# Kernel optimization log

Hardware: AMD Instinct MI355X
Metric: run time of the kernel (lower is better)

## Reference

```python
import jax, jax.numpy as jnp
import numpy as np

B, S, C, H, D = 4, 2048, 512, 8, 64
EPS = 1e-5
SCALE = D ** -0.5


def layer_norm(x, w, b):
    m = jnp.mean(x, axis=-1, keepdims=True)
    v = jnp.var(x, axis=-1, keepdims=True)
    return (x - m) * jax.lax.rsqrt(v + EPS) * w + b


def setup_inputs() -> dict:
    key = jax.random.key(0)
    ks = jax.random.split(key, 7)
    s = 0.02
    return {
        "x": jax.random.normal(ks[0], (B, S, C), jnp.float32),
        "Wq": jax.random.normal(ks[1], (C, H * D), jnp.float32) * s,
        "Wk": jax.random.normal(ks[2], (C, H * D), jnp.float32) * s,
        "Wv": jax.random.normal(ks[3], (C, H * D), jnp.float32) * s,
        "Wo": jax.random.normal(ks[4], (H * D, C), jnp.float32) * s,
        "ln1_w": jnp.ones((C,), jnp.float32), "ln1_b": jnp.zeros((C,), jnp.float32),
        "ff_ln1_w": jnp.ones((C,), jnp.float32), "ff_ln1_b": jnp.zeros((C,), jnp.float32),
        "ff_w1": jax.random.normal(ks[5], (C, C), jnp.float32) * s, "ff_b1": jnp.zeros((C,), jnp.float32),
        "ff_ln2_w": jnp.ones((C,), jnp.float32), "ff_ln2_b": jnp.zeros((C,), jnp.float32),
        "ff_w2": jax.random.normal(ks[6], (C, C), jnp.float32) * s, "ff_b2": jnp.zeros((C,), jnp.float32),
        "ln2_w": jnp.ones((C,), jnp.float32), "ln2_b": jnp.zeros((C,), jnp.float32),
    }


def causal_attention(x, Wq, Wk, Wv, Wo):
    # Mathematically identical to the bucketed memory-efficient attention:
    # online-softmax bucketing changes compute order, not the result.
    q = (x @ Wq).reshape(B, S, H, D).transpose(0, 2, 1, 3)  # [B,H,S,D]
    k = (x @ Wk).reshape(B, S, H, D).transpose(0, 2, 1, 3)
    v = (x @ Wv).reshape(B, S, H, D).transpose(0, 2, 1, 3)
    scores = jnp.einsum('bhqd,bhkd->bhqk', q, k) * SCALE  # [B,H,S,S]
    causal = jnp.tril(jnp.ones((S, S), bool))
    scores = jnp.where(causal, scores, jnp.finfo(scores.dtype).min)
    attn = jax.nn.softmax(scores, axis=-1)
    out = jnp.einsum('bhqk,bhkd->bhqd', attn, v)
    out = out.transpose(0, 2, 1, 3).reshape(B, S, H * D)
    return out @ Wo


def reference(x, Wq, Wk, Wv, Wo, ln1_w, ln1_b, ff_ln1_w, ff_ln1_b, ff_w1, ff_b1,
              ff_ln2_w, ff_ln2_b, ff_w2, ff_b2, ln2_w, ln2_b):
    a = causal_attention(x, Wq, Wk, Wv, Wo)
    x_ln = layer_norm(a + x, ln1_w, ln1_b)
    h = layer_norm(x_ln, ff_ln1_w, ff_ln1_b) @ ff_w1 + ff_b1
    h = layer_norm(h, ff_ln2_w, ff_ln2_b) @ ff_w2 + ff_b2
    return layer_norm(h + x_ln, ln2_w, ln2_b)
```

## Files before the change

kernel.cpp:

```cpp
#include <hip/hip_runtime.h>

#define B_ 4
#define S_ 2048
#define C_ 512
#define H_ 8
#define D_ 64
#define M_ 8192

typedef short s8v __attribute__((ext_vector_type(8)));
typedef short s4v __attribute__((ext_vector_type(4)));
typedef float f4v __attribute__((ext_vector_type(4)));
typedef unsigned short u16;
typedef unsigned int u32;

__device__ __forceinline__ u16 f2b(float f) {
    u32 u = __builtin_bit_cast(u32, f);
    u = u + 0x7fffu + ((u >> 16) & 1u);
    return (u16)(u >> 16);
}

__device__ __forceinline__ void b2f8(const s8v v, float* f) {
    #pragma unroll
    for (int k = 0; k < 8; ++k)
        f[k] = __builtin_bit_cast(float, (u32)(u16)v[k] << 16);
}

__device__ __forceinline__ void gl2lds16(const void* g, void* l) {
    __builtin_amdgcn_global_load_lds(
        (const __attribute__((address_space(1))) void*)g,
        (__attribute__((address_space(3))) void*)l, 16, 0, 0);
}

__global__ __launch_bounds__(256) void conv_k(const float* __restrict__ s,
                                              u16* __restrict__ d) {
    const int i = (blockIdx.x * 256 + threadIdx.x) * 4;
    const float4 v = *(const float4*)&s[i];
    ushort4 o;
    o.x = f2b(v.x); o.y = f2b(v.y); o.z = f2b(v.z); o.w = f2b(v.w);
    *(ushort4*)&d[i] = o;
}

__global__ __launch_bounds__(256) void trconv6_k(const float* __restrict__ s0,
                                                 const float* __restrict__ s1,
                                                 const float* __restrict__ s2,
                                                 const float* __restrict__ s3,
                                                 const float* __restrict__ s4,
                                                 const float* __restrict__ s5,
                                                 u16* __restrict__ d0,
                                                 u16* __restrict__ d1,
                                                 u16* __restrict__ d2,
                                                 u16* __restrict__ d3,
                                                 u16* __restrict__ d4,
                                                 u16* __restrict__ d5)
{
    const float* W; u16* Wt;
    switch (blockIdx.z) {
        case 0: W = s0; Wt = d0; break;
        case 1: W = s1; Wt = d1; break;
        case 2: W = s2; Wt = d2; break;
        case 3: W = s3; Wt = d3; break;
        case 4: W = s4; Wt = d4; break;
        default: W = s5; Wt = d5; break;
    }
    __shared__ float t[32][33];
    const int tx = threadIdx.x & 31, ty = threadIdx.x >> 5;
    const int n0 = blockIdx.x * 32, k0 = blockIdx.y * 32;
    #pragma unroll
    for (int i = 0; i < 4; ++i)
        t[ty + i * 8][tx] = W[(size_t)(k0 + ty + i * 8) * C_ + n0 + tx];
    __syncthreads();
    #pragma unroll
    for (int i = 0; i < 4; ++i)
        Wt[(size_t)(n0 + ty + i * 8) * C_ + k0 + tx] = f2b(t[tx][ty + i * 8]);
}

template <bool OB>
__global__ __launch_bounds__(256) void gemm_k(const u16* __restrict__ A,
                                              const u16* __restrict__ Bt,
                                              const float* __restrict__ bias,
                                              void* __restrict__ outv)
{
    __shared__ u16 As[2][4][16][32];
    __shared__ u16 Bs[2][4][16][32];
    const int tid = threadIdx.x;
    const int lane = tid & 63, w = tid >> 6;
    const int q4 = lane >> 4, l16 = lane & 15;
    const int wr = w >> 1, wc = w & 1;
    const int bm = blockIdx.y * 64, bn = blockIdx.x * 64;
    const int lr = lane >> 2, lc = (lane & 3) * 8;

    f4v acc[2][2];
    #pragma unroll
    for (int i = 0; i < 2; ++i)
        #pragma unroll
        for (int j = 0; j < 2; ++j) acc[i][j] = (f4v){0.f, 0.f, 0.f, 0.f};

    gl2lds16(A  + (size_t)(bm + w * 16 + lr) * C_ + lc, (char*)As + w * 1024);
    gl2lds16(Bt + (size_t)(bn + w * 16 + lr) * C_ + lc, (char*)Bs + w * 1024);

    for (int kt = 0; kt < 16; ++kt) {
        __syncthreads();
        const int buf = kt & 1;
        if (kt < 15) {
            const int nb = buf ^ 1, k0 = (kt + 1) * 32;
            gl2lds16(A  + (size_t)(bm + w * 16 + lr) * C_ + k0 + lc,
                     (char*)As + nb * 4096 + w * 1024);
            gl2lds16(Bt + (size_t)(bn + w * 16 + lr) * C_ + k0 + lc,
                     (char*)Bs + nb * 4096 + w * 1024);
        }
        s8v a[2], bfr[2];
        #pragma unroll
        for (int i = 0; i < 2; ++i) {
            const int row = wr * 32 + i * 16 + l16;
            a[i] = *(const s8v*)&As[buf][row >> 4][row & 15][q4 * 8];
        }
        #pragma unroll
        for (int j = 0; j < 2; ++j) {
            const int row = wc * 32 + j * 16 + l16;
            bfr[j] = *(const s8v*)&Bs[buf][row >> 4][row & 15][q4 * 8];
        }
        #pragma unroll
        for (int i = 0; i < 2; ++i)
            #pragma unroll
            for (int j = 0; j < 2; ++j)
                acc[i][j] = __builtin_amdgcn_mfma_f32_16x16x32_bf16(a[i], bfr[j], acc[i][j], 0, 0, 0);
    }

    #pragma unroll
    for (int j = 0; j < 2; ++j) {
        const int n = bn + wc * 32 + j * 16 + l16;
        const float bj = bias ? bias[n] : 0.0f;
        #pragma unroll
        for (int i = 0; i < 2; ++i) {
            const int m = bm + wr * 32 + i * 16 + q4 * 4;
            #pragma unroll
            for (int reg = 0; reg < 4; ++reg) {
                const float vv = acc[i][j][reg] + bj;
                if constexpr (OB) ((u16*)outv)[(size_t)(m + reg) * C_ + n] = f2b(vv);
                else              ((float*)outv)[(size_t)(m + reg) * C_ + n] = vv;
            }
        }
    }
}

__global__ __launch_bounds__(256) void qkv_k(const u16* __restrict__ A,
                                             const u16* __restrict__ Wq,
                                             const u16* __restrict__ Wk,
                                             const u16* __restrict__ Wv,
                                             u16* __restrict__ oq,
                                             u16* __restrict__ ok,
                                             u16* __restrict__ ovt)
{
    __shared__ u16 As[2][4][16][32];
    __shared__ u16 Bs[2][4][16][32];
    const int tid = threadIdx.x;
    const int lane = tid & 63, w = tid >> 6;
    const int q4 = lane >> 4, l16 = lane & 15;
    const int wr = w >> 1, wc = w & 1;
    const int nt = blockIdx.x, which = nt >> 3;
    const u16* Bt = which == 0 ? Wq : (which == 1 ? Wk : Wv);
    const int bm = blockIdx.y * 64, bn = (nt & 7) * 64;
    const int lr = lane >> 2, lc = (lane & 3) * 8;

    f4v acc[2][2];
    #pragma unroll
    for (int i = 0; i < 2; ++i)
        #pragma unroll
        for (int j = 0; j < 2; ++j) acc[i][j] = (f4v){0.f, 0.f, 0.f, 0.f};

    gl2lds16(A  + (size_t)(bm + w * 16 + lr) * C_ + lc, (char*)As + w * 1024);
    gl2lds16(Bt + (size_t)(bn + w * 16 + lr) * C_ + lc, (char*)Bs + w * 1024);

    for (int kt = 0; kt < 16; ++kt) {
        __syncthreads();
        const int buf = kt & 1;
        if (kt < 15) {
            const int nb = buf ^ 1, k0 = (kt + 1) * 32;
            gl2lds16(A  + (size_t)(bm + w * 16 + lr) * C_ + k0 + lc,
                     (char*)As + nb * 4096 + w * 1024);
            gl2lds16(Bt + (size_t)(bn + w * 16 + lr) * C_ + k0 + lc,
                     (char*)Bs + nb * 4096 + w * 1024);
        }
        s8v a[2], bfr[2];
        #pragma unroll
        for (int i = 0; i < 2; ++i) {
            const int row = wr * 32 + i * 16 + l16;
            a[i] = *(const s8v*)&As[buf][row >> 4][row & 15][q4 * 8];
        }
        #pragma unroll
        for (int j = 0; j < 2; ++j) {
            const int row = wc * 32 + j * 16 + l16;
            bfr[j] = *(const s8v*)&Bs[buf][row >> 4][row & 15][q4 * 8];
        }
        #pragma unroll
        for (int i = 0; i < 2; ++i)
            #pragma unroll
            for (int j = 0; j < 2; ++j)
                acc[i][j] = __builtin_amdgcn_mfma_f32_16x16x32_bf16(a[i], bfr[j], acc[i][j], 0, 0, 0);
    }

    if (which == 0) {
        #pragma unroll
        for (int j = 0; j < 2; ++j) {
            const int n = bn + wc * 32 + j * 16 + l16;
            #pragma unroll
            for (int i = 0; i < 2; ++i) {
                const int m = bm + wr * 32 + i * 16 + q4 * 4;
                #pragma unroll
                for (int reg = 0; reg < 4; ++reg)
                    oq[(size_t)(m + reg) * C_ + n] = f2b(acc[i][j][reg]);
            }
        }
    } else if (which == 1) {
        #pragma unroll
        for (int j = 0; j < 2; ++j) {
            const int n = bn + wc * 32 + j * 16 + l16;
            const int nswz = (n & ~31) | ((((n >> 3) & 3) ^ q4) << 3) | (n & 7);
            #pragma unroll
            for (int i = 0; i < 2; ++i) {
                const int m = bm + wr * 32 + i * 16 + q4 * 4;
                #pragma unroll
                for (int reg = 0; reg < 4; ++reg)
                    ok[(size_t)(m + reg) * C_ + nswz] = f2b(acc[i][j][reg]);
            }
        }
    } else {
        const int bglob = bm >> 11;
        const int sbase = bm & (S_ - 1);
        #pragma unroll
        for (int j = 0; j < 2; ++j) {
            const int n = bn + wc * 32 + j * 16 + l16;
            const int h = n >> 6, d = n & 63;
            u16* vrow = ovt + ((size_t)(bglob * H_ + h) * D_ + d) * S_;
            const int xw = d & 7;
            #pragma unroll
            for (int i = 0; i < 2; ++i) {
                const int s = sbase + wr * 32 + i * 16 + q4 * 4;
                const int pg = ((s & 31) >> 2) ^ xw;
                s4v pv;
                #pragma unroll
                for (int reg = 0; reg < 4; ++reg) pv[reg] = (short)f2b(acc[i][j][reg]);
                *(s4v*)&vrow[(s & ~31) + (pg << 2)] = pv;
            }
        }
    }
}

__global__ __launch_bounds__(256) void ln2xb_k(const u16* __restrict__ in,
                                               const float* __restrict__ res,
                                               const float* __restrict__ w1,
                                               const float* __restrict__ b1,
                                               const float* __restrict__ w2,
                                               const float* __restrict__ b2,
                                               u16* __restrict__ out1,
                                               u16* __restrict__ out2)
{
    const int lane = threadIdx.x & 63;
    const int row  = blockIdx.x * 4 + (threadIdx.x >> 6);
    const size_t off = (size_t)row * C_ + lane * 8;
    float v[8];
    b2f8(*(const s8v*)&in[off], v);
    {
        const float4 r0 = *(const float4*)&res[off];
        const float4 r1 = *(const float4*)&res[off + 4];
        v[0] += r0.x; v[1] += r0.y; v[2] += r0.z; v[3] += r0.w;
        v[4] += r1.x; v[5] += r1.y; v[6] += r1.z; v[7] += r1.w;
    }
    float s = 0.f, ss = 0.f;
    #pragma unroll
    for (int k = 0; k < 8; ++k) { s += v[k]; ss += v[k] * v[k]; }
    #pragma unroll
    for (int o = 32; o >= 1; o >>= 1) { s += __shfl_xor(s, o); ss += __shfl_xor(ss, o); }
    float mean = s * (1.0f / C_);
    float rstd = rsqrtf(ss * (1.0f / C_) - mean * mean + 1e-5f);

    const float4 wA0 = *(const float4*)&w1[lane * 8];
    const float4 wA1 = *(const float4*)&w1[lane * 8 + 4];
    const float4 bA0 = *(const float4*)&b1[lane * 8];
    const float4 bA1 = *(const float4*)&b1[lane * 8 + 4];
    const float wA[8] = {wA0.x, wA0.y, wA0.z, wA0.w, wA1.x, wA1.y, wA1.z, wA1.w};
    const float bA[8] = {bA0.x, bA0.y, bA0.z, bA0.w, bA1.x, bA1.y, bA1.z, bA1.w};
    float y[8];
    s8v o1;
    #pragma unroll
    for (int k = 0; k < 8; ++k) {
        y[k] = (v[k] - mean) * rstd * wA[k] + bA[k];
        o1[k] = (short)f2b(y[k]);
    }
    *(s8v*)&out1[off] = o1;

    s = 0.f; ss = 0.f;
    #pragma unroll
    for (int k = 0; k < 8; ++k) { s += y[k]; ss += y[k] * y[k]; }
    #pragma unroll
    for (int o = 32; o >= 1; o >>= 1) { s += __shfl_xor(s, o); ss += __shfl_xor(ss, o); }
    mean = s * (1.0f / C_);
    rstd = rsqrtf(ss * (1.0f / C_) - mean * mean + 1e-5f);

    const float4 wB0 = *(const float4*)&w2[lane * 8];
    const float4 wB1 = *(const float4*)&w2[lane * 8 + 4];
    const float4 bB0 = *(const float4*)&b2[lane * 8];
    const float4 bB1 = *(const float4*)&b2[lane * 8 + 4];
    const float wB[8] = {wB0.x, wB0.y, wB0.z, wB0.w, wB1.x, wB1.y, wB1.z, wB1.w};
    const float bB[8] = {bB0.x, bB0.y, bB0.z, bB0.w, bB1.x, bB1.y, bB1.z, bB1.w};
    s8v o2;
    #pragma unroll
    for (int k = 0; k < 8; ++k)
        o2[k] = (short)f2b((y[k] - mean) * rstd * wB[k] + bB[k]);
    *(s8v*)&out2[off] = o2;
}

__global__ __launch_bounds__(256) void lnb_k(const u16* __restrict__ in,
                                             const float* __restrict__ w,
                                             const float* __restrict__ bb,
                                             u16* __restrict__ out)
{
    const int lane = threadIdx.x & 63;
    const int row  = blockIdx.x * 4 + (threadIdx.x >> 6);
    const size_t off = (size_t)row * C_ + lane * 8;
    float v[8];
    b2f8(*(const s8v*)&in[off], v);
    float s = 0.f, ss = 0.f;
    #pragma unroll
    for (int k = 0; k < 8; ++k) { s += v[k]; ss += v[k] * v[k]; }
    #pragma unroll
    for (int o = 32; o >= 1; o >>= 1) { s += __shfl_xor(s, o); ss += __shfl_xor(ss, o); }
    const float mean = s * (1.0f / C_);
    const float rstd = rsqrtf(ss * (1.0f / C_) - mean * mean + 1e-5f);
    const float4 w0 = *(const float4*)&w[lane * 8];
    const float4 w1 = *(const float4*)&w[lane * 8 + 4];
    const float4 b0 = *(const float4*)&bb[lane * 8];
    const float4 b1 = *(const float4*)&bb[lane * 8 + 4];
    const float wv[8] = {w0.x, w0.y, w0.z, w0.w, w1.x, w1.y, w1.z, w1.w};
    const float bv[8] = {b0.x, b0.y, b0.z, b0.w, b1.x, b1.y, b1.z, b1.w};
    s8v o;
    #pragma unroll
    for (int k = 0; k < 8; ++k)
        o[k] = (short)f2b((v[k] - mean) * rstd * wv[k] + bv[k]);
    *(s8v*)&out[off] = o;
}

__global__ __launch_bounds__(256) void lnfin_k(const u16* __restrict__ in,
                                               const u16* __restrict__ res,
                                               const float* __restrict__ w,
                                               const float* __restrict__ bb,
                                               float* __restrict__ out)
{
    const int lane = threadIdx.x & 63;
    const int row  = blockIdx.x * 4 + (threadIdx.x >> 6);
    const size_t off = (size_t)row * C_ + lane * 8;
    float v[8], r[8];
    b2f8(*(const s8v*)&in[off], v);
    b2f8(*(const s8v*)&res[off], r);
    #pragma unroll
    for (int k = 0; k < 8; ++k) v[k] += r[k];
    float s = 0.f, ss = 0.f;
    #pragma unroll
    for (int k = 0; k < 8; ++k) { s += v[k]; ss += v[k] * v[k]; }
    #pragma unroll
    for (int o = 32; o >= 1; o >>= 1) { s += __shfl_xor(s, o); ss += __shfl_xor(ss, o); }
    const float mean = s * (1.0f / C_);
    const float rstd = rsqrtf(ss * (1.0f / C_) - mean * mean + 1e-5f);
    const float4 w0 = *(const float4*)&w[lane * 8];
    const float4 w1 = *(const float4*)&w[lane * 8 + 4];
    const float4 b0 = *(const float4*)&bb[lane * 8];
    const float4 b1 = *(const float4*)&bb[lane * 8 + 4];
    const float wv[8] = {w0.x, w0.y, w0.z, w0.w, w1.x, w1.y, w1.z, w1.w};
    const float bv[8] = {b0.x, b0.y, b0.z, b0.w, b1.x, b1.y, b1.z, b1.w};
    float4 o0, o1;
    o0.x = (v[0] - mean) * rstd * wv[0] + bv[0];
    o0.y = (v[1] - mean) * rstd * wv[1] + bv[1];
    o0.z = (v[2] - mean) * rstd * wv[2] + bv[2];
    o0.w = (v[3] - mean) * rstd * wv[3] + bv[3];
    o1.x = (v[4] - mean) * rstd * wv[4] + bv[4];
    o1.y = (v[5] - mean) * rstd * wv[5] + bv[5];
    o1.z = (v[6] - mean) * rstd * wv[6] + bv[6];
    o1.w = (v[7] - mean) * rstd * wv[7] + bv[7];
    *(float4*)&out[off]     = o0;
    *(float4*)&out[off + 4] = o1;
}

__global__ __launch_bounds__(256) void attn_k(const u16* __restrict__ Q,
                                              const u16* __restrict__ K,
                                              const u16* __restrict__ Vt,
                                              u16* __restrict__ O)
{
    __shared__ u16 Ks[2][2][64][32];
    __shared__ u16 Vs[2][2][64][32];
    const int tid = threadIdx.x;
    const int lane = tid & 63, w = tid >> 6;
    const int q4 = lane >> 4, l16 = lane & 15;
    const int x = blockIdx.x, h = blockIdx.y, b = blockIdx.z;
    const int qb = (x & 1) ? 31 - (x >> 1) : (x >> 1);
    const size_t base  = ((size_t)b * S_) * C_ + h * D_;
    const size_t basev = ((size_t)(b * H_ + h)) * D_ * S_;
    const int lr = lane >> 2, lc = (lane & 3) * 8;
    const int kq = (q4 ^ ((l16 >> 2) & 3)) * 8;

    s8v qf[2];
    #pragma unroll
    for (int kh = 0; kh < 2; ++kh)
        qf[kh] = *(const s8v*)&Q[base + (size_t)(qb * 64 + w * 16 + l16) * C_ + kh * 32 + q4 * 8];

    #pragma unroll
    for (int r = 0; r < 2; ++r) {
        const int seg = r * 4 + w;
        const int row = (seg & 3) * 16 + lr;
        const int kh = seg >> 2;
        gl2lds16(K  + base  + (size_t)row * C_ + kh * 32 + lc, (char*)Ks + seg * 1024);
        gl2lds16(Vt + basev + (size_t)row * S_ + kh * 32 + lc, (char*)Vs + seg * 1024);
    }

    f4v o[4];
    float lp[4] = {0.f, 0.f, 0.f, 0.f};
    #pragma unroll
    for (int j = 0; j < 4; ++j) o[j] = (f4v){0.f, 0.f, 0.f, 0.f};

    const int qrow = w * 16 + l16;
    for (int kb = 0; kb <= qb; ++kb) {
        __syncthreads();
        const int buf = kb & 1;
        if (kb < qb) {
            const int nb = buf ^ 1, kn = kb + 1;
            #pragma unroll
            for (int r = 0; r < 2; ++r) {
                const int seg = r * 4 + w;
                const int row = (seg & 3) * 16 + lr;
                const int kh = seg >> 2;
                gl2lds16(K  + base  + (size_t)(kn * 64 + row) * C_ + kh * 32 + lc,
                         (char*)Ks + nb * 8192 + seg * 1024);
                gl2lds16(Vt + basev + (size_t)row * S_ + kn * 64 + kh * 32 + lc,
                         (char*)Vs + nb * 8192 + seg * 1024);
            }
        }

        f4v sc[4];
        #pragma unroll
        for (int j = 0; j < 4; ++j) sc[j] = (f4v){0.f, 0.f, 0.f, 0.f};
        #pragma unroll
        for (int kh = 0; kh < 2; ++kh) {
            #pragma unroll
            for (int j = 0; j < 4; ++j) {
                const s8v kf = *(const s8v*)&Ks[buf][kh][j * 16 + l16][kq];
                sc[j] = __builtin_amdgcn_mfma_f32_16x16x32_bf16(kf, qf[kh], sc[j], 0, 0, 0);
            }
        }

        const bool diag = (kb == qb);
        s4v pa[4];
        #pragma unroll
        for (int j = 0; j < 4; ++j) {
            float ps = 0.0f;
            #pragma unroll
            for (int reg = 0; reg < 4; ++reg) {
                float t = fmaf(sc[j][reg], 0.18033688011112043f, -11.541560327111707f);
                if (diag && (j * 16 + q4 * 4 + reg) > qrow) t = -128.0f;
                const float p = exp2f(t);
                ps += p;
                pa[j][reg] = (short)(__builtin_bit_cast(u32, p) >> 16);
            }
            lp[j] += ps;
        }

        #pragma unroll
        for (int c = 0; c < 4; ++c) {
            const int gh = (((c & 1) * 4 + q4) ^ (l16 & 7)) * 4;
            #pragma unroll
            for (int dj = 0; dj < 4; ++dj) {
                const s4v vb = *(const s4v*)&Vs[buf][c >> 1][dj * 16 + l16][gh];
                o[dj] = __builtin_amdgcn_mfma_f32_16x16x16bf16_1k(pa[c], vb, o[dj], 0, 0, 0);
            }
        }
    }

    float lt = (lp[0] + lp[1]) + (lp[2] + lp[3]);
    lt += __shfl_xor(lt, 16);
    lt += __shfl_xor(lt, 32);
    #pragma unroll
    for (int reg = 0; reg < 4; ++reg) {
        const float inv = 1.0f / __shfl(lt, q4 * 4 + reg);
        const size_t rowoff = base + (size_t)(qb * 64 + w * 16 + q4 * 4 + reg) * C_;
        #pragma unroll
        for (int dj = 0; dj < 4; ++dj)
            O[rowoff + dj * 16 + l16] = f2b(o[dj][reg] * inv);
    }
}

extern "C" void kernel_launch(void* const* d_in, const int* in_sizes, int n_in,
                              void* d_out, int out_size, void* d_ws, size_t ws_size,
                              hipStream_t stream)
{
    const float* x       = (const float*)d_in[0];
    const float* Wq      = (const float*)d_in[1];
    const float* Wk      = (const float*)d_in[2];
    const float* Wv      = (const float*)d_in[3];
    const float* Wo      = (const float*)d_in[4];
    const float* ln1_w   = (const float*)d_in[5];
    const float* ln1_b   = (const float*)d_in[6];
    const float* ffln1_w = (const float*)d_in[7];
    const float* ffln1_b = (const float*)d_in[8];
    const float* ff_w1   = (const float*)d_in[9];
    const float* ff_b1   = (const float*)d_in[10];
    const float* ffln2_w = (const float*)d_in[11];
    const float* ffln2_b = (const float*)d_in[12];
    const float* ff_w2   = (const float*)d_in[13];
    const float* ff_b2   = (const float*)d_in[14];
    const float* ln2_w   = (const float*)d_in[15];
    const float* ln2_b   = (const float*)d_in[16];
    float* out = (float*)d_out;

    const size_t MC = (size_t)M_ * C_;
    const size_t WW = (size_t)C_ * C_;
    u16* xb   = (u16*)d_ws;
    u16* WqT  = xb + MC;
    u16* WkT  = WqT + WW;
    u16* WvT  = WkT + WW;
    u16* WoT  = WvT + WW;
    u16* W1T  = WoT + WW;
    u16* W2T  = W1T + WW;
    u16* qbuf = W2T + WW;
    u16* kbuf = qbuf + MC;
    u16* vbuf = kbuf + MC;
    u16* vtbuf= vbuf + MC;
    u16*  abuf = xb;
    u16*  tf   = qbuf;
    u16*  xln  = vbuf;

    const dim3 gg(C_ / 64, M_ / 64);
    const dim3 gq(24, M_ / 64);
    const dim3 ga(32, H_, B_);
    const dim3 gt(16, 16, 6);
    const int  gl = M_ / 4;

    conv_k<<<MC / 1024, 256, 0, stream>>>(x, xb);
    trconv6_k<<<gt, 256, 0, stream>>>(Wq, Wk, Wv, Wo, ff_w1, ff_w2,
                                      WqT, WkT, WvT, WoT, W1T, W2T);

    qkv_k<<<gq, 256, 0, stream>>>(xb, WqT, WkT, WvT, qbuf, kbuf, vtbuf);
    attn_k<<<ga, 256, 0, stream>>>(qbuf, kbuf, vtbuf, abuf);

    gemm_k<true><<<gg, 256, 0, stream>>>(abuf, WoT, nullptr, tf);
    ln2xb_k<<<gl, 256, 0, stream>>>(tf, x, ln1_w, ln1_b, ffln1_w, ffln1_b,
                                    xln, xb);
    gemm_k<true><<<gg, 256, 0, stream>>>(xb, W1T, ff_b1, tf);
    lnb_k<<<gl, 256, 0, stream>>>(tf, ffln2_w, ffln2_b, xb);
    gemm_k<true><<<gg, 256, 0, stream>>>(xb, W2T, ff_b2, tf);
    lnfin_k<<<gl, 256, 0, stream>>>(tf, xln, ln2_w, ln2_b, out);
}
```

Measured before the change: 263.5 us.

## Merge prep kernels, schedule attention longest-first, split diagonal softmax path

```diff
diff --git a/kernel.cpp b/kernel.cpp
--- a/kernel.cpp
+++ b/kernel.cpp
@@ -31,30 +31,35 @@
         (__attribute__((address_space(3))) void*)l, 16, 0, 0);
 }
 
-__global__ __launch_bounds__(256) void conv_k(const float* __restrict__ s,
-                                              u16* __restrict__ d) {
-    const int i = (blockIdx.x * 256 + threadIdx.x) * 4;
-    const float4 v = *(const float4*)&s[i];
-    ushort4 o;
-    o.x = f2b(v.x); o.y = f2b(v.y); o.z = f2b(v.z); o.w = f2b(v.w);
-    *(ushort4*)&d[i] = o;
-}
-
-__global__ __launch_bounds__(256) void trconv6_k(const float* __restrict__ s0,
-                                                 const float* __restrict__ s1,
-                                                 const float* __restrict__ s2,
-                                                 const float* __restrict__ s3,
-                                                 const float* __restrict__ s4,
-                                                 const float* __restrict__ s5,
-                                                 u16* __restrict__ d0,
-                                                 u16* __restrict__ d1,
-                                                 u16* __restrict__ d2,
-                                                 u16* __restrict__ d3,
-                                                 u16* __restrict__ d4,
-                                                 u16* __restrict__ d5)
-{
+__global__ __launch_bounds__(256) void prep_k(const float* __restrict__ x,
+                                              u16* __restrict__ xb,
+                                              const float* __restrict__ s0,
+                                              const float* __restrict__ s1,
+                                              const float* __restrict__ s2,
+                                              const float* __restrict__ s3,
+                                              const float* __restrict__ s4,
+                                              const float* __restrict__ s5,
+                                              u16* __restrict__ d0,
+                                              u16* __restrict__ d1,
+                                              u16* __restrict__ d2,
+                                              u16* __restrict__ d3,
+                                              u16* __restrict__ d4,
+                                              u16* __restrict__ d5)
+{
+    __shared__ float t[32][33];
+    const int bx = blockIdx.x;
+    if (bx < 4096) {
+        const int i = (bx * 256 + (int)threadIdx.x) * 4;
+        const float4 v = *(const float4*)&x[i];
+        ushort4 o;
+        o.x = f2b(v.x); o.y = f2b(v.y); o.z = f2b(v.z); o.w = f2b(v.w);
+        *(ushort4*)&xb[i] = o;
+        return;
+    }
+    const int tb = bx - 4096;
+    const int z = tb >> 8, rem = tb & 255;
     const float* W; u16* Wt;
-    switch (blockIdx.z) {
+    switch (z) {
         case 0: W = s0; Wt = d0; break;
         case 1: W = s1; Wt = d1; break;
         case 2: W = s2; Wt = d2; break;
@@ -62,9 +67,8 @@
         case 4: W = s4; Wt = d4; break;
         default: W = s5; Wt = d5; break;
     }
-    __shared__ float t[32][33];
     const int tx = threadIdx.x & 31, ty = threadIdx.x >> 5;
-    const int n0 = blockIdx.x * 32, k0 = blockIdx.y * 32;
+    const int n0 = (rem & 15) * 32, k0 = (rem >> 4) * 32;
     #pragma unroll
     for (int i = 0; i < 4; ++i)
         t[ty + i * 8][tx] = W[(size_t)(k0 + ty + i * 8) * C_ + n0 + tx];
@@ -390,8 +394,8 @@
     const int tid = threadIdx.x;
     const int lane = tid & 63, w = tid >> 6;
     const int q4 = lane >> 4, l16 = lane & 15;
-    const int x = blockIdx.x, h = blockIdx.y, b = blockIdx.z;
-    const int qb = (x & 1) ? 31 - (x >> 1) : (x >> 1);
+    const int h = blockIdx.y, b = blockIdx.z;
+    const int qb = 31 - (int)blockIdx.x;
     const size_t base  = ((size_t)b * S_) * C_ + h * D_;
     const size_t basev = ((size_t)(b * H_ + h)) * D_ * S_;
     const int lr = lane >> 2, lc = (lane & 3) * 8;
@@ -446,20 +450,34 @@
             }
         }
 
-        const bool diag = (kb == qb);
         s4v pa[4];
-        #pragma unroll
-        for (int j = 0; j < 4; ++j) {
-            float ps = 0.0f;
-            #pragma unroll
-            for (int reg = 0; reg < 4; ++reg) {
-                float t = fmaf(sc[j][reg], 0.18033688011112043f, -11.541560327111707f);
-                if (diag && (j * 16 + q4 * 4 + reg) > qrow) t = -128.0f;
-                const float p = exp2f(t);
-                ps += p;
-                pa[j][reg] = (short)(__builtin_bit_cast(u32, p) >> 16);
-            }
-            lp[j] += ps;
+        if (kb == qb) {
+            #pragma unroll
+            for (int j = 0; j < 4; ++j) {
+                float ps = 0.0f;
+                #pragma unroll
+                for (int reg = 0; reg < 4; ++reg) {
+                    float t = fmaf(sc[j][reg], 0.18033688011112043f, -11.541560327111707f);
+                    if ((j * 16 + q4 * 4 + reg) > qrow) t = -128.0f;
+                    const float p = exp2f(t);
+                    ps += p;
+                    pa[j][reg] = (short)(__builtin_bit_cast(u32, p) >> 16);
+                }
+                lp[j] += ps;
+            }
+        } else {
+            #pragma unroll
+            for (int j = 0; j < 4; ++j) {
+                float ps = 0.0f;
+                #pragma unroll
+                for (int reg = 0; reg < 4; ++reg) {
+                    const float p = exp2f(fmaf(sc[j][reg], 0.18033688011112043f,
+                                               -11.541560327111707f));
+                    ps += p;
+                    pa[j][reg] = (short)(__builtin_bit_cast(u32, p) >> 16);
+                }
+                lp[j] += ps;
+            }
         }
 
         #pragma unroll
@@ -529,12 +547,10 @@
     const dim3 gg(C_ / 64, M_ / 64);
     const dim3 gq(24, M_ / 64);
     const dim3 ga(32, H_, B_);
-    const dim3 gt(16, 16, 6);
     const int  gl = M_ / 4;
 
-    conv_k<<<MC / 1024, 256, 0, stream>>>(x, xb);
-    trconv6_k<<<gt, 256, 0, stream>>>(Wq, Wk, Wv, Wo, ff_w1, ff_w2,
-                                      WqT, WkT, WvT, WoT, W1T, W2T);
+    prep_k<<<5632, 256, 0, stream>>>(x, xb, Wq, Wk, Wv, Wo, ff_w1, ff_w2,
+                                     WqT, WkT, WvT, WoT, W1T, W2T);
 
     qkv_k<<<gq, 256, 0, stream>>>(xb, WqT, WkT, WvT, qbuf, kbuf, vtbuf);
     attn_k<<<ga, 256, 0, stream>>>(qbuf, kbuf, vtbuf, abuf);
```

After: 258.4 us. Within noise of the previous version (-1.9%).
